# Performance work log

Measured on AMD Instinct MI355X. Metric: run time of the kernel, lower is better.

Reference implementation:

```python
import jax, jax.numpy as jnp
import numpy as np

NUM_FEAT = 512
NUM_HEAD = 8
DEPTH = NUM_FEAT // NUM_HEAD
B, S = 2, 4096


def setup_inputs() -> dict:
    key = jax.random.key(0)
    ks = jax.random.split(key, 12)
    sc = 1.0 / np.sqrt(NUM_FEAT)
    inp = {
        "q": jax.random.normal(ks[0], (B, S, NUM_FEAT), jnp.float32),
        "k": jax.random.normal(ks[1], (B, S, NUM_FEAT), jnp.float32),
        "v": jax.random.normal(ks[2], (B, S, NUM_FEAT), jnp.float32),
        # causal mask: 1 where attention is disallowed (upper triangle), additive style
        "mask": jnp.triu(jnp.ones((S, S), jnp.float32), k=1)[None, None, :, :],
        "wq": jax.random.normal(ks[3], (NUM_FEAT, NUM_FEAT), jnp.float32) * sc,
        "bq": jnp.zeros((NUM_FEAT,), jnp.float32),
        "wk": jax.random.normal(ks[4], (NUM_FEAT, NUM_FEAT), jnp.float32) * sc,
        "bk": jnp.zeros((NUM_FEAT,), jnp.float32),
        "wv": jax.random.normal(ks[5], (NUM_FEAT, NUM_FEAT), jnp.float32) * sc,
        "bv": jnp.zeros((NUM_FEAT,), jnp.float32),
        "wo": jax.random.normal(ks[6], (NUM_FEAT, NUM_FEAT), jnp.float32) * sc,
        "bo": jnp.zeros((NUM_FEAT,), jnp.float32),
    }
    return inp


def _split_heads(x):
    b, s, _ = x.shape
    return x.reshape(b, s, NUM_HEAD, DEPTH).transpose(0, 2, 1, 3)  # [B,H,S,D]


def reference(q, k, v, mask, wq, bq, wk, bk, wv, bv, wo, bo):
    qh = _split_heads(q @ wq + bq)
    kh = _split_heads(k @ wk + bk)
    vh = _split_heads(v @ wv + bv)
    # scaled dot-product attention with materialized [B,H,S,S] scores
    logits = jnp.einsum("bhqd,bhkd->bhqk", qh, kh) / jnp.sqrt(jnp.float32(DEPTH))
    logits = logits + mask * (-1e9)
    weights = jax.nn.softmax(logits, axis=-1)
    attn = jnp.einsum("bhqk,bhkd->bhqd", weights, vh)
    concat = attn.transpose(0, 2, 1, 3).reshape(q.shape[0], -1, NUM_FEAT)
    return concat @ wo + bo
```

## Files before the change

### kernel.cpp

```cpp
#include <hip/hip_runtime.h>
#include <hip/hip_bf16.h>
#include <stdint.h>

#define NB 2
#define NS 4096
#define NF 512
#define NH 8
#define ND 64
#define NM (NB * NS)

typedef __attribute__((ext_vector_type(8))) short bf16x8;
typedef __attribute__((ext_vector_type(4))) float f32x4;
typedef __attribute__((ext_vector_type(16))) float f32x16;

static __device__ __forceinline__ unsigned short f2bf(float f) {
    union { float f; uint32_t u; } x; x.f = f;
    uint32_t u = x.u;
    u += 0x7FFFu + ((u >> 16) & 1u);
    return (unsigned short)(u >> 16);
}

static __device__ __forceinline__ void load_lds16(const void* g, void* l) {
    __builtin_amdgcn_global_load_lds(
        (const __attribute__((address_space(1))) void*)g,
        (__attribute__((address_space(3))) void*)l,
        16, 0, 0);
}

__global__ void convert_all(const float* __restrict__ q, const float* __restrict__ k,
                            const float* __restrict__ v,
                            unsigned short* __restrict__ qb, unsigned short* __restrict__ kb,
                            unsigned short* __restrict__ vb,
                            const float* __restrict__ wq, const float* __restrict__ wk,
                            const float* __restrict__ wv, const float* __restrict__ wo,
                            unsigned short* __restrict__ o0, unsigned short* __restrict__ o1,
                            unsigned short* __restrict__ o2, unsigned short* __restrict__ o3) {
    int i0 = blockIdx.x * blockDim.x + threadIdx.x;
    int stride = gridDim.x * blockDim.x;
    const int n4 = (NB * NS * NF) / 4;
    for (int i = i0; i < n4; i += stride) {
        float4 a = ((const float4*)q)[i];
        float4 b = ((const float4*)k)[i];
        float4 c = ((const float4*)v)[i];
        ushort4 oa, ob, oc;
        oa.x = f2bf(a.x); oa.y = f2bf(a.y); oa.z = f2bf(a.z); oa.w = f2bf(a.w);
        ob.x = f2bf(b.x); ob.y = f2bf(b.y); ob.z = f2bf(b.z); ob.w = f2bf(b.w);
        oc.x = f2bf(c.x); oc.y = f2bf(c.y); oc.z = f2bf(c.z); oc.w = f2bf(c.w);
        ((ushort4*)qb)[i] = oa;
        ((ushort4*)kb)[i] = ob;
        ((ushort4*)vb)[i] = oc;
    }
    for (int i = i0; i < 4 * NF * NF; i += stride) {
        int w = i >> 18;
        int off = i & (NF * NF - 1);
        int r = off >> 9;
        int c = off & (NF - 1);
        const float* src = (w == 0) ? wq : (w == 1) ? wk : (w == 2) ? wv : wo;
        unsigned short* dst = (w == 0) ? o0 : (w == 1) ? o1 : (w == 2) ? o2 : o3;
        dst[c * NF + r] = f2bf(src[off]);
    }
}

__launch_bounds__(256, 2)
__global__ void proj_qkv(const unsigned short* __restrict__ Aq,
                         const unsigned short* __restrict__ Ak,
                         const unsigned short* __restrict__ Av,
                         const unsigned short* __restrict__ WqT,
                         const unsigned short* __restrict__ WkT,
                         const unsigned short* __restrict__ WvT,
                         const float* __restrict__ bq, const float* __restrict__ bk,
                         const float* __restrict__ bv,
                         unsigned short* __restrict__ Qh, unsigned short* __restrict__ Kh,
                         unsigned short* __restrict__ VTs) {
    __shared__ unsigned short smem[2 * 128 * 64];
    unsigned short* As = smem;
    unsigned short* Bs = smem + 128 * 64;

    const int mode = blockIdx.z;
    const unsigned short* A  = (mode == 0) ? Aq : (mode == 1) ? Ak : Av;
    const unsigned short* WT = (mode == 0) ? WqT : (mode == 1) ? WkT : WvT;
    const float* bias        = (mode == 0) ? bq : (mode == 1) ? bk : bv;

    const int t = threadIdx.x;
    const int wid = t >> 6;
    const int lane = t & 63;
    const int l15 = lane & 15;
    const int lhi = lane >> 4;
    const int m0 = blockIdx.x * 128;
    const int n0 = blockIdx.y * 128;
    const int wm = (wid >> 1) * 64;
    const int wn = (wid & 1) * 64;

    const int srow = t >> 3;
    const int scol = ((t & 7) * 16) ^ ((srow & 7) << 4);

    const f32x4 zero4 = {0.f, 0.f, 0.f, 0.f};
    f32x4 acc[4][4];
#pragma unroll
    for (int i = 0; i < 4; ++i)
#pragma unroll
        for (int j = 0; j < 4; ++j) acc[i][j] = zero4;

    for (int k0 = 0; k0 < NF; k0 += 64) {
        __syncthreads();
#pragma unroll
        for (int i = 0; i < 4; ++i) {
            const char* sa = (const char*)A + ((size_t)(m0 + i * 32 + srow) * NF + k0) * 2 + scol;
            load_lds16(sa, (char*)As + i * 4096 + wid * 1024);
            const char* sb = (const char*)WT + ((size_t)(n0 + i * 32 + srow) * NF + k0) * 2 + scol;
            load_lds16(sb, (char*)Bs + i * 4096 + wid * 1024);
        }
        asm volatile("s_waitcnt vmcnt(0)" ::: "memory");
        __syncthreads();

#pragma unroll
        for (int ks = 0; ks < 2; ++ks) {
            bf16x8 af[4], bfr[4];
#pragma unroll
            for (int i = 0; i < 4; ++i) {
                int ra = wm + i * 16 + l15;
                int ca = (ks * 64 + lhi * 16) ^ ((ra & 7) << 4);
                af[i] = *(const bf16x8*)((const char*)As + ra * 128 + ca);
                int rb = wn + i * 16 + l15;
                int cb = (ks * 64 + lhi * 16) ^ ((rb & 7) << 4);
                bfr[i] = *(const bf16x8*)((const char*)Bs + rb * 128 + cb);
            }
#pragma unroll
            for (int mi = 0; mi < 4; ++mi)
#pragma unroll
                for (int ni = 0; ni < 4; ++ni)
                    acc[mi][ni] = __builtin_amdgcn_mfma_f32_16x16x32_bf16(af[mi], bfr[ni], acc[mi][ni], 0, 0, 0);
        }
    }

#pragma unroll
    for (int ni = 0; ni < 4; ++ni) {
        int col = n0 + wn + ni * 16 + l15;
        float bv2 = bias[col];
#pragma unroll
        for (int mi = 0; mi < 4; ++mi) {
#pragma unroll
            for (int r = 0; r < 4; ++r) {
                int row = m0 + wm + mi * 16 + lhi * 4 + r;
                float val = acc[mi][ni][r] + bv2;
                int b = row >> 12, s = row & (NS - 1);
                int hh = col >> 6, d = col & (ND - 1);
                if (mode == 0) {
                    val *= 0.125f;
                    Qh[((size_t)(b * NH + hh) * NS + s) * ND + d] = f2bf(val);
                } else if (mode == 1) {
                    Kh[((size_t)(b * NH + hh) * NS + s) * ND + d] = f2bf(val);
                } else {
                    VTs[((size_t)(b * NH + hh) * ND + d) * NS + s] = f2bf(val);
                }
            }
        }
    }
}

__launch_bounds__(256, 2)
__global__ void proj_o(const unsigned short* __restrict__ A,
                       const unsigned short* __restrict__ WT,
                       const float* __restrict__ bias,
                       float* __restrict__ Out) {
    __shared__ unsigned short smem[2 * 128 * 64];
    unsigned short* As = smem;
    unsigned short* Bs = smem + 128 * 64;

    const int t = threadIdx.x;
    const int wid = t >> 6;
    const int lane = t & 63;
    const int l15 = lane & 15;
    const int lhi = lane >> 4;
    const int m0 = blockIdx.x * 128;
    const int n0 = blockIdx.y * 128;
    const int wm = (wid >> 1) * 64;
    const int wn = (wid & 1) * 64;

    const int srow = t >> 3;
    const int scol = ((t & 7) * 16) ^ ((srow & 7) << 4);

    const f32x4 zero4 = {0.f, 0.f, 0.f, 0.f};
    f32x4 acc[4][4];
#pragma unroll
    for (int i = 0; i < 4; ++i)
#pragma unroll
        for (int j = 0; j < 4; ++j) acc[i][j] = zero4;

    for (int k0 = 0; k0 < NF; k0 += 64) {
        __syncthreads();
#pragma unroll
        for (int i = 0; i < 4; ++i) {
            const char* sa = (const char*)A + ((size_t)(m0 + i * 32 + srow) * NF + k0) * 2 + scol;
            load_lds16(sa, (char*)As + i * 4096 + wid * 1024);
            const char* sb = (const char*)WT + ((size_t)(n0 + i * 32 + srow) * NF + k0) * 2 + scol;
            load_lds16(sb, (char*)Bs + i * 4096 + wid * 1024);
        }
        asm volatile("s_waitcnt vmcnt(0)" ::: "memory");
        __syncthreads();

#pragma unroll
        for (int ks = 0; ks < 2; ++ks) {
            bf16x8 af[4], bfr[4];
#pragma unroll
            for (int i = 0; i < 4; ++i) {
                int ra = wm + i * 16 + l15;
                int ca = (ks * 64 + lhi * 16) ^ ((ra & 7) << 4);
                af[i] = *(const bf16x8*)((const char*)As + ra * 128 + ca);
                int rb = wn + i * 16 + l15;
                int cb = (ks * 64 + lhi * 16) ^ ((rb & 7) << 4);
                bfr[i] = *(const bf16x8*)((const char*)Bs + rb * 128 + cb);
            }
#pragma unroll
            for (int mi = 0; mi < 4; ++mi)
#pragma unroll
                for (int ni = 0; ni < 4; ++ni)
                    acc[mi][ni] = __builtin_amdgcn_mfma_f32_16x16x32_bf16(af[mi], bfr[ni], acc[mi][ni], 0, 0, 0);
        }
    }

#pragma unroll
    for (int ni = 0; ni < 4; ++ni) {
        int col = n0 + wn + ni * 16 + l15;
        float bv2 = bias[col];
#pragma unroll
        for (int mi = 0; mi < 4; ++mi)
#pragma unroll
            for (int r = 0; r < 4; ++r) {
                int row = m0 + wm + mi * 16 + lhi * 4 + r;
                Out[(size_t)row * NF + col] = acc[mi][ni][r] + bv2;
            }
    }
}

__launch_bounds__(128, 2)
__global__ void attn_fused(const unsigned short* __restrict__ Qh,
                           const unsigned short* __restrict__ Kh,
                           const unsigned short* __restrict__ VT,
                           unsigned short* __restrict__ Cc) {
    __shared__ unsigned short smem[16384];

    const int t = threadIdx.x;
    const int wid = t >> 6;
    const int lane = t & 63;
    const int l31 = lane & 31;
    const int h = lane >> 5;
    const int qt = 63 - (int)blockIdx.x;
    const int hh = blockIdx.y, b = blockIdx.z;
    const int q0 = qt * 64;
    const size_t bh = (size_t)b * NH + hh;
    const char* Qp = (const char*)(Qh + bh * NS * ND);
    const char* Kp = (const char*)(Kh + bh * NS * ND);
    const char* Vp = (const char*)(VT + bh * (size_t)ND * NS);

    const int qrow = q0 + wid * 32 + l31;
    bf16x8 qf[4];
#pragma unroll
    for (int kc = 0; kc < 4; ++kc)
        qf[kc] = *(const bf16x8*)(Qp + (size_t)qrow * 128 + kc * 32 + h * 16);

    f32x16 o[2];
#pragma unroll
    for (int r = 0; r < 16; ++r) { o[0][r] = 0.f; o[1][r] = 0.f; }
    float m_run = -1e30f, l_run = 0.f;

    const int srow = lane >> 3;
    const int scol = ((lane & 7) * 16) ^ ((srow & 7) << 4);
    const size_t koff = (size_t)srow * 128 + scol;
    const size_t voff = (size_t)srow * (NS * 2) + scol;

    auto STAGE = [&](int buf, int kv0) {
        char* lk = (char*)smem + buf * 16384;
        if (wid == 0) {
            const char* g = Kp + (size_t)kv0 * 128 + koff;
#pragma unroll
            for (int i = 0; i < 8; ++i)
                load_lds16(g + i * 1024, lk + i * 1024);
        } else {
            const char* g = Vp + (size_t)kv0 * 2 + voff;
            char* lv = lk + 8192;
#pragma unroll
            for (int i = 0; i < 8; ++i)
                load_lds16(g + (size_t)i * 8 * (NS * 2), lv + i * 1024);
        }
    };

    const int nkv = qt + 1;
    const int sw = (l31 & 7) << 4;
    STAGE(0, 0);
    int cur = 0;

    for (int kt = 0; kt < nkv; ++kt) {
        if (kt + 1 < nkv) {
            STAGE(cur ^ 1, (kt + 1) * 64);
            asm volatile("s_waitcnt vmcnt(8)" ::: "memory");
        } else {
            asm volatile("s_waitcnt vmcnt(0)" ::: "memory");
        }
        __builtin_amdgcn_s_barrier();
        __builtin_amdgcn_sched_barrier(0);

        const char* Kb = (const char*)smem + cur * 16384;
        const char* Vb = Kb + 8192;

        f32x16 sT[2];
#pragma unroll
        for (int r = 0; r < 16; ++r) { sT[0][r] = 0.f; sT[1][r] = 0.f; }
#pragma unroll
        for (int kvi = 0; kvi < 2; ++kvi) {
            const int row = kvi * 32 + l31;
#pragma unroll
            for (int kc = 0; kc < 4; ++kc) {
                bf16x8 kf = *(const bf16x8*)(Kb + row * 128 + ((kc * 32 + h * 16) ^ sw));
                sT[kvi] = __builtin_amdgcn_mfma_f32_32x32x16_bf16(kf, qf[kc], sT[kvi], 0, 0, 0);
            }
        }

        if (kt == qt) {
#pragma unroll
            for (int kvi = 0; kvi < 2; ++kvi)
#pragma unroll
                for (int r = 0; r < 16; ++r) {
                    int kv = kt * 64 + kvi * 32 + (r & 3) + ((r >> 2) << 3) + h * 4;
                    if (kv > qrow) sT[kvi][r] = -1e30f;
                }
        }

        float pm = -1e30f;
#pragma unroll
        for (int kvi = 0; kvi < 2; ++kvi)
#pragma unroll
            for (int r = 0; r < 16; ++r) pm = fmaxf(pm, sT[kvi][r]);
        pm = fmaxf(pm, __shfl_xor(pm, 32));

        if (__ballot(pm > m_run + 8.0f) != 0ull) {
            float mnew = fmaxf(m_run, pm);
            float a = __expf(m_run - mnew);
            m_run = mnew;
            l_run *= a;
#pragma unroll
            for (int di = 0; di < 2; ++di)
#pragma unroll
                for (int r = 0; r < 16; ++r) o[di][r] *= a;
        }
        float rs = 0.f;
#pragma unroll
        for (int kvi = 0; kvi < 2; ++kvi)
#pragma unroll
            for (int r = 0; r < 16; ++r) {
                float p = __expf(sT[kvi][r] - m_run);
                sT[kvi][r] = p;
                rs += p;
            }
        rs += __shfl_xor(rs, 32);
        l_run += rs;

        unsigned int w[2][8];
#pragma unroll
        for (int kvi = 0; kvi < 2; ++kvi)
#pragma unroll
            for (int i = 0; i < 8; ++i)
                w[kvi][i] = (unsigned int)f2bf(sT[kvi][2 * i]) |
                            ((unsigned int)f2bf(sT[kvi][2 * i + 1]) << 16);

        union FB { unsigned int u[4]; bf16x8 v; };
        bf16x8 pf[4];
#pragma unroll
        for (int ck = 0; ck < 4; ++ck) {
            const int kvi = ck >> 1, pb = (ck & 1) * 4;
            unsigned int aSrc = h ? w[kvi][pb + 0] : w[kvi][pb + 2];
            unsigned int bSrc = h ? w[kvi][pb + 1] : w[kvi][pb + 3];
            unsigned int sA = (unsigned int)__shfl_xor((int)aSrc, 32);
            unsigned int sB = (unsigned int)__shfl_xor((int)bSrc, 32);
            FB f;
            f.u[0] = (h == 0) ? w[kvi][pb + 0] : sA;
            f.u[1] = (h == 0) ? w[kvi][pb + 1] : sB;
            f.u[2] = (h == 0) ? sA : w[kvi][pb + 2];
            f.u[3] = (h == 0) ? sB : w[kvi][pb + 3];
            pf[ck] = f.v;
        }

#pragma unroll
        for (int di = 0; di < 2; ++di) {
            const int row = di * 32 + l31;
#pragma unroll
            for (int ck = 0; ck < 4; ++ck) {
                bf16x8 vf = *(const bf16x8*)(Vb + row * 128 + ((ck * 32 + h * 16) ^ sw));
                o[di] = __builtin_amdgcn_mfma_f32_32x32x16_bf16(vf, pf[ck], o[di], 0, 0, 0);
            }
        }

        __builtin_amdgcn_sched_barrier(0);
        __builtin_amdgcn_s_barrier();
        cur ^= 1;
    }

    float inv = 1.0f / l_run;
    size_t obase = ((size_t)b * NS + qrow) * NF + hh * ND;
#pragma unroll
    for (int di = 0; di < 2; ++di)
#pragma unroll
        for (int tq = 0; tq < 4; ++tq) {
            ushort4 pk;
            pk.x = f2bf(o[di][4 * tq + 0] * inv);
            pk.y = f2bf(o[di][4 * tq + 1] * inv);
            pk.z = f2bf(o[di][4 * tq + 2] * inv);
            pk.w = f2bf(o[di][4 * tq + 3] * inv);
            *(ushort4*)(Cc + obase + di * 32 + tq * 8 + h * 4) = pk;
        }
}

extern "C" void kernel_launch(void* const* d_in, const int* in_sizes, int n_in,
                              void* d_out, int out_size, void* d_ws, size_t ws_size,
                              hipStream_t stream) {
    const float* q = (const float*)d_in[0];
    const float* k = (const float*)d_in[1];
    const float* v = (const float*)d_in[2];
    const float* wq = (const float*)d_in[4];
    const float* bq = (const float*)d_in[5];
    const float* wk = (const float*)d_in[6];
    const float* bk = (const float*)d_in[7];
    const float* wv = (const float*)d_in[8];
    const float* bv = (const float*)d_in[9];
    const float* wo = (const float*)d_in[10];
    const float* bo = (const float*)d_in[11];

    const size_t MB = 1u << 20;
    char* ws = (char*)d_ws;
    unsigned short* qb  = (unsigned short*)(ws);
    unsigned short* kb  = (unsigned short*)(ws + 8 * MB);
    unsigned short* vb  = (unsigned short*)(ws + 16 * MB);
    unsigned short* wqT = (unsigned short*)(ws + 24 * MB);
    unsigned short* wkT = (unsigned short*)(ws + 24 * MB + 512 * 1024);
    unsigned short* wvT = (unsigned short*)(ws + 25 * MB);
    unsigned short* woT = (unsigned short*)(ws + 25 * MB + 512 * 1024);
    unsigned short* Qh  = (unsigned short*)(ws + 26 * MB);
    unsigned short* Kh  = (unsigned short*)(ws + 34 * MB);
    unsigned short* VTs = (unsigned short*)(ws + 42 * MB);

    convert_all<<<dim3(2048), dim3(256), 0, stream>>>(q, k, v, qb, kb, vb,
                                                      wq, wk, wv, wo, wqT, wkT, wvT, woT);

    proj_qkv<<<dim3(NM / 128, NF / 128, 3), dim3(256), 0, stream>>>(
        qb, kb, vb, wqT, wkT, wvT, bq, bk, bv, Qh, Kh, VTs);

    attn_fused<<<dim3(64, NH, NB), dim3(128), 0, stream>>>(Qh, Kh, VTs, qb );

    proj_o<<<dim3(NM / 128, NF / 128), dim3(256), 0, stream>>>(qb, woT, bo, (float*)d_out);
}
```

Baseline: 310.8 us.

## Split attention KV loop across two wave pairs and double-buffer projection GEMMs

The attention kernel now runs 256 threads per block, with two wave pairs each processing alternating KV tiles. Their partial softmax states (max, sum, output) are merged through LDS at the end, which shortens the serial causal loop per block. Both projection GEMMs get a double-buffered LDS pipeline with partial vmcnt waits so the next tile loads while the current one computes. The output projection also moves to 64-row tiles for more blocks. The costs are extra LDS per block, which may limit occupancy, and a merge epilogue with its own synchronisation.

```diff
diff --git a/kernel.cpp b/kernel.cpp
--- a/kernel.cpp
+++ b/kernel.cpp
@@ -72,9 +72,7 @@
                          const float* __restrict__ bv,
                          unsigned short* __restrict__ Qh, unsigned short* __restrict__ Kh,
                          unsigned short* __restrict__ VTs) {
-    __shared__ unsigned short smem[2 * 128 * 64];
-    unsigned short* As = smem;
-    unsigned short* Bs = smem + 128 * 64;
+    __shared__ char smem[65536];
 
     const int mode = blockIdx.z;
     const unsigned short* A  = (mode == 0) ? Aq : (mode == 1) ? Ak : Av;
@@ -101,18 +99,32 @@
 #pragma unroll
         for (int j = 0; j < 4; ++j) acc[i][j] = zero4;
 
-    for (int k0 = 0; k0 < NF; k0 += 64) {
-        __syncthreads();
+    auto STAGE = [&](int buf, int k0) {
+        char* As = smem + buf * 32768;
+        char* Bs = As + 16384;
 #pragma unroll
         for (int i = 0; i < 4; ++i) {
             const char* sa = (const char*)A + ((size_t)(m0 + i * 32 + srow) * NF + k0) * 2 + scol;
-            load_lds16(sa, (char*)As + i * 4096 + wid * 1024);
+            load_lds16(sa, As + i * 4096 + wid * 1024);
             const char* sb = (const char*)WT + ((size_t)(n0 + i * 32 + srow) * NF + k0) * 2 + scol;
-            load_lds16(sb, (char*)Bs + i * 4096 + wid * 1024);
-        }
-        asm volatile("s_waitcnt vmcnt(0)" ::: "memory");
-        __syncthreads();
-
+            load_lds16(sb, Bs + i * 4096 + wid * 1024);
+        }
+    };
+
+    STAGE(0, 0);
+    int cur = 0;
+    for (int kt = 0; kt < 8; ++kt) {
+        if (kt < 7) {
+            STAGE(cur ^ 1, (kt + 1) * 64);
+            asm volatile("s_waitcnt vmcnt(8)" ::: "memory");
+        } else {
+            asm volatile("s_waitcnt vmcnt(0)" ::: "memory");
+        }
+        __builtin_amdgcn_s_barrier();
+        __builtin_amdgcn_sched_barrier(0);
+
+        const char* As = smem + cur * 32768;
+        const char* Bs = As + 16384;
 #pragma unroll
         for (int ks = 0; ks < 2; ++ks) {
             bf16x8 af[4], bfr[4];
@@ -120,10 +132,10 @@
             for (int i = 0; i < 4; ++i) {
                 int ra = wm + i * 16 + l15;
                 int ca = (ks * 64 + lhi * 16) ^ ((ra & 7) << 4);
-                af[i] = *(const bf16x8*)((const char*)As + ra * 128 + ca);
+                af[i] = *(const bf16x8*)(As + ra * 128 + ca);
                 int rb = wn + i * 16 + l15;
                 int cb = (ks * 64 + lhi * 16) ^ ((rb & 7) << 4);
-                bfr[i] = *(const bf16x8*)((const char*)Bs + rb * 128 + cb);
+                bfr[i] = *(const bf16x8*)(Bs + rb * 128 + cb);
             }
 #pragma unroll
             for (int mi = 0; mi < 4; ++mi)
@@ -131,6 +143,9 @@
                 for (int ni = 0; ni < 4; ++ni)
                     acc[mi][ni] = __builtin_amdgcn_mfma_f32_16x16x32_bf16(af[mi], bfr[ni], acc[mi][ni], 0, 0, 0);
         }
+        __builtin_amdgcn_sched_barrier(0);
+        __builtin_amdgcn_s_barrier();
+        cur ^= 1;
     }
 
 #pragma unroll
@@ -163,60 +178,81 @@
                        const unsigned short* __restrict__ WT,
                        const float* __restrict__ bias,
                        float* __restrict__ Out) {
-    __shared__ unsigned short smem[2 * 128 * 64];
-    unsigned short* As = smem;
-    unsigned short* Bs = smem + 128 * 64;
+    __shared__ char smem[49152];
 
     const int t = threadIdx.x;
     const int wid = t >> 6;
     const int lane = t & 63;
     const int l15 = lane & 15;
     const int lhi = lane >> 4;
-    const int m0 = blockIdx.x * 128;
+    const int m0 = blockIdx.x * 64;
     const int n0 = blockIdx.y * 128;
-    const int wm = (wid >> 1) * 64;
+    const int wm = (wid >> 1) * 32;
     const int wn = (wid & 1) * 64;
 
     const int srow = t >> 3;
     const int scol = ((t & 7) * 16) ^ ((srow & 7) << 4);
 
     const f32x4 zero4 = {0.f, 0.f, 0.f, 0.f};
-    f32x4 acc[4][4];
-#pragma unroll
-    for (int i = 0; i < 4; ++i)
+    f32x4 acc[2][4];
+#pragma unroll
+    for (int i = 0; i < 2; ++i)
 #pragma unroll
         for (int j = 0; j < 4; ++j) acc[i][j] = zero4;
 
-    for (int k0 = 0; k0 < NF; k0 += 64) {
-        __syncthreads();
+    auto STAGE = [&](int buf, int k0) {
+        char* As = smem + buf * 24576;
+        char* Bs = As + 8192;
+#pragma unroll
+        for (int i = 0; i < 2; ++i) {
+            const char* sa = (const char*)A + ((size_t)(m0 + i * 32 + srow) * NF + k0) * 2 + scol;
+            load_lds16(sa, As + i * 4096 + wid * 1024);
+        }
 #pragma unroll
         for (int i = 0; i < 4; ++i) {
-            const char* sa = (const char*)A + ((size_t)(m0 + i * 32 + srow) * NF + k0) * 2 + scol;
-            load_lds16(sa, (char*)As + i * 4096 + wid * 1024);
             const char* sb = (const char*)WT + ((size_t)(n0 + i * 32 + srow) * NF + k0) * 2 + scol;
-            load_lds16(sb, (char*)Bs + i * 4096 + wid * 1024);
-        }
-        asm volatile("s_waitcnt vmcnt(0)" ::: "memory");
-        __syncthreads();
-
+            load_lds16(sb, Bs + i * 4096 + wid * 1024);
+        }
+    };
+
+    STAGE(0, 0);
+    int cur = 0;
+    for (int kt = 0; kt < 8; ++kt) {
+        if (kt < 7) {
+            STAGE(cur ^ 1, (kt + 1) * 64);
+            asm volatile("s_waitcnt vmcnt(6)" ::: "memory");
+        } else {
+            asm volatile("s_waitcnt vmcnt(0)" ::: "memory");
+        }
+        __builtin_amdgcn_s_barrier();
+        __builtin_amdgcn_sched_barrier(0);
+
+        const char* As = smem + cur * 24576;
+        const char* Bs = As + 8192;
 #pragma unroll
         for (int ks = 0; ks < 2; ++ks) {
-            bf16x8 af[4], bfr[4];
-#pragma unroll
-            for (int i = 0; i < 4; ++i) {
+            bf16x8 af[2], bfr[4];
+#pragma unroll
+            for (int i = 0; i < 2; ++i) {
                 int ra = wm + i * 16 + l15;
                 int ca = (ks * 64 + lhi * 16) ^ ((ra & 7) << 4);
-                af[i] = *(const bf16x8*)((const char*)As + ra * 128 + ca);
+                af[i] = *(const bf16x8*)(As + ra * 128 + ca);
+            }
+#pragma unroll
+            for (int i = 0; i < 4; ++i) {
                 int rb = wn + i * 16 + l15;
                 int cb = (ks * 64 + lhi * 16) ^ ((rb & 7) << 4);
-                bfr[i] = *(const bf16x8*)((const char*)Bs + rb * 128 + cb);
-            }
-#pragma unroll
-            for (int mi = 0; mi < 4; ++mi)
+                bfr[i] = *(const bf16x8*)(Bs + rb * 128 + cb);
+            }
+#pragma unroll
+            for (int mi = 0; mi < 2; ++mi)
 #pragma unroll
                 for (int ni = 0; ni < 4; ++ni)
                     acc[mi][ni] = __builtin_amdgcn_mfma_f32_16x16x32_bf16(af[mi], bfr[ni], acc[mi][ni], 0, 0, 0);
         }
+        __builtin_amdgcn_sched_barrier(0);
+        __builtin_amdgcn_s_barrier();
+        cur ^= 1;
     }
 
 #pragma unroll
@@ -224,7 +260,7 @@
         int col = n0 + wn + ni * 16 + l15;
         float bv2 = bias[col];
 #pragma unroll
-        for (int mi = 0; mi < 4; ++mi)
+        for (int mi = 0; mi < 2; ++mi)
 #pragma unroll
             for (int r = 0; r < 4; ++r) {
                 int row = m0 + wm + mi * 16 + lhi * 4 + r;
@@ -233,15 +269,17 @@
     }
 }
 
-__launch_bounds__(128, 2)
+__launch_bounds__(256, 2)
 __global__ void attn_fused(const unsigned short* __restrict__ Qh,
                            const unsigned short* __restrict__ Kh,
                            const unsigned short* __restrict__ VT,
                            unsigned short* __restrict__ Cc) {
-    __shared__ unsigned short smem[16384];
+    __shared__ char smem[65536];
 
     const int t = threadIdx.x;
     const int wid = t >> 6;
+    const int pair = wid >> 1;
+    const int a = wid & 1;
     const int lane = t & 63;
     const int l31 = lane & 31;
     const int h = lane >> 5;
@@ -253,7 +291,7 @@
     const char* Kp = (const char*)(Kh + bh * NS * ND);
     const char* Vp = (const char*)(VT + bh * (size_t)ND * NS);
 
-    const int qrow = q0 + wid * 32 + l31;
+    const int qrow = q0 + a * 32 + l31;
     bf16x8 qf[4];
 #pragma unroll
     for (int kc = 0; kc < 4; ++kc)
@@ -268,31 +306,34 @@
     const int scol = ((lane & 7) * 16) ^ ((srow & 7) << 4);
     const size_t koff = (size_t)srow * 128 + scol;
     const size_t voff = (size_t)srow * (NS * 2) + scol;
+    char* pbase = smem + pair * 32768;
 
     auto STAGE = [&](int buf, int kv0) {
-        char* lk = (char*)smem + buf * 16384;
-        if (wid == 0) {
+        char* dst = pbase + buf * 16384;
+        if (a == 0) {
             const char* g = Kp + (size_t)kv0 * 128 + koff;
 #pragma unroll
             for (int i = 0; i < 8; ++i)
-                load_lds16(g + i * 1024, lk + i * 1024);
+                load_lds16(g + i * 1024, dst + i * 1024);
         } else {
             const char* g = Vp + (size_t)kv0 * 2 + voff;
-            char* lv = lk + 8192;
+            char* lv = dst + 8192;
 #pragma unroll
             for (int i = 0; i < 8; ++i)
                 load_lds16(g + (size_t)i * 8 * (NS * 2), lv + i * 1024);
         }
     };
 
-    const int nkv = qt + 1;
+    const int myC = (qt + 2 - pair) >> 1;
+    const int R = (qt + 2) >> 1;
     const int sw = (l31 & 7) << 4;
-    STAGE(0, 0);
+
+    if (0 < myC) STAGE(0, pair * 64);
     int cur = 0;
 
-    for (int kt = 0; kt < nkv; ++kt) {
-        if (kt + 1 < nkv) {
-            STAGE(cur ^ 1, (kt + 1) * 64);
+    for (int j = 0; j < R; ++j) {
+        if (j + 1 < myC) {
+            STAGE(cur ^ 1, (2 * (j + 1) + pair) * 64);
             asm volatile("s_waitcnt vmcnt(8)" ::: "memory");
         } else {
             asm volatile("s_waitcnt vmcnt(0)" ::: "memory");
@@ -300,93 +341,96 @@
         __builtin_amdgcn_s_barrier();
         __builtin_amdgcn_sched_barrier(0);
 
-        const char* Kb = (const char*)smem + cur * 16384;
-        const char* Vb = Kb + 8192;
-
-        f32x16 sT[2];
-#pragma unroll
-        for (int r = 0; r < 16; ++r) { sT[0][r] = 0.f; sT[1][r] = 0.f; }
-#pragma unroll
-        for (int kvi = 0; kvi < 2; ++kvi) {
-            const int row = kvi * 32 + l31;
-#pragma unroll
-            for (int kc = 0; kc < 4; ++kc) {
-                bf16x8 kf = *(const bf16x8*)(Kb + row * 128 + ((kc * 32 + h * 16) ^ sw));
-                sT[kvi] = __builtin_amdgcn_mfma_f32_32x32x16_bf16(kf, qf[kc], sT[kvi], 0, 0, 0);
-            }
-        }
-
-        if (kt == qt) {
+        if (j < myC) {
+            const int kt = 2 * j + pair;
+            const char* Kb = pbase + cur * 16384;
+            const char* Vb = Kb + 8192;
+
+            f32x16 sT[2];
+#pragma unroll
+            for (int r = 0; r < 16; ++r) { sT[0][r] = 0.f; sT[1][r] = 0.f; }
+#pragma unroll
+            for (int kvi = 0; kvi < 2; ++kvi) {
+                const int row = kvi * 32 + l31;
+#pragma unroll
+                for (int kc = 0; kc < 4; ++kc) {
+                    bf16x8 kf = *(const bf16x8*)(Kb + row * 128 + ((kc * 32 + h * 16) ^ sw));
+                    sT[kvi] = __builtin_amdgcn_mfma_f32_32x32x16_bf16(kf, qf[kc], sT[kvi], 0, 0, 0);
+                }
+            }
+
+            if (kt == qt) {
+#pragma unroll
+                for (int kvi = 0; kvi < 2; ++kvi)
+#pragma unroll
+                    for (int r = 0; r < 16; ++r) {
+                        int kv = kt * 64 + kvi * 32 + (r & 3) + ((r >> 2) << 3) + h * 4;
+                        if (kv > qrow) sT[kvi][r] = -1e30f;
+                    }
+            }
+
+            float pm = -1e30f;
 #pragma unroll
             for (int kvi = 0; kvi < 2; ++kvi)
 #pragma unroll
+                for (int r = 0; r < 16; ++r) pm = fmaxf(pm, sT[kvi][r]);
+            pm = fmaxf(pm, __shfl_xor(pm, 32));
+
+            if (__ballot(pm > m_run + 8.0f) != 0ull) {
+                float mnew = fmaxf(m_run, pm);
+                float sc = __expf(m_run - mnew);
+                m_run = mnew;
+                l_run *= sc;
+#pragma unroll
+                for (int di = 0; di < 2; ++di)
+#pragma unroll
+                    for (int r = 0; r < 16; ++r) o[di][r] *= sc;
+            }
+            float rs = 0.f;
+#pragma unroll
+            for (int kvi = 0; kvi < 2; ++kvi)
+#pragma unroll
                 for (int r = 0; r < 16; ++r) {
-                    int kv = kt * 64 + kvi * 32 + (r & 3) + ((r >> 2) << 3) + h * 4;
-                    if (kv > qrow) sT[kvi][r] = -1e30f;
+                    float p = __expf(sT[kvi][r] - m_run);
+                    sT[kvi][r] = p;
+                    rs += p;
                 }
-        }
-
-        float pm = -1e30f;
-#pragma unroll
-        for (int kvi = 0; kvi < 2; ++kvi)
-#pragma unroll
-            for (int r = 0; r < 16; ++r) pm = fmaxf(pm, sT[kvi][r]);
-        pm = fmaxf(pm, __shfl_xor(pm, 32));
-
-        if (__ballot(pm > m_run + 8.0f) != 0ull) {
-            float mnew = fmaxf(m_run, pm);
-            float a = __expf(m_run - mnew);
-            m_run = mnew;
-            l_run *= a;
-#pragma unroll
-            for (int di = 0; di < 2; ++di)
-#pragma unroll
-                for (int r = 0; r < 16; ++r) o[di][r] *= a;
-        }
-        float rs = 0.f;
-#pragma unroll
-        for (int kvi = 0; kvi < 2; ++kvi)
-#pragma unroll
-            for (int r = 0; r < 16; ++r) {
-                float p = __expf(sT[kvi][r] - m_run);
-                sT[kvi][r] = p;
-                rs += p;
-            }
-        rs += __shfl_xor(rs, 32);
-        l_run += rs;
-
-        unsigned int w[2][8];
-#pragma unroll
-        for (int kvi = 0; kvi < 2; ++kvi)
-#pragma unroll
-            for (int i = 0; i < 8; ++i)
-                w[kvi][i] = (unsigned int)f2bf(sT[kvi][2 * i]) |
-                            ((unsigned int)f2bf(sT[kvi][2 * i + 1]) << 16);
-
-        union FB { unsigned int u[4]; bf16x8 v; };
-        bf16x8 pf[4];
-#pragma unroll
-        for (int ck = 0; ck < 4; ++ck) {
-            const int kvi = ck >> 1, pb = (ck & 1) * 4;
-            unsigned int aSrc = h ? w[kvi][pb + 0] : w[kvi][pb + 2];
-            unsigned int bSrc = h ? w[kvi][pb + 1] : w[kvi][pb + 3];
-            unsigned int sA = (unsigned int)__shfl_xor((int)aSrc, 32);
-            unsigned int sB = (unsigned int)__shfl_xor((int)bSrc, 32);
-            FB f;
-            f.u[0] = (h == 0) ? w[kvi][pb + 0] : sA;
-            f.u[1] = (h == 0) ? w[kvi][pb + 1] : sB;
-            f.u[2] = (h == 0) ? sA : w[kvi][pb + 2];
-            f.u[3] = (h == 0) ? sB : w[kvi][pb + 3];
-            pf[ck] = f.v;
-        }
-
-#pragma unroll
-        for (int di = 0; di < 2; ++di) {
-            const int row = di * 32 + l31;
+            rs += __shfl_xor(rs, 32);
+            l_run += rs;
+
+            unsigned int w[2][8];
+#pragma unroll
+            for (int kvi = 0; kvi < 2; ++kvi)
+#pragma unroll
+                for (int i = 0; i < 8; ++i)
+                    w[kvi][i] = (unsigned int)f2bf(sT[kvi][2 * i]) |
+                                ((unsigned int)f2bf(sT[kvi][2 * i + 1]) << 16);
+
+            union FB { unsigned int u[4]; bf16x8 v; };
+            bf16x8 pf[4];
 #pragma unroll
             for (int ck = 0; ck < 4; ++ck) {
-                bf16x8 vf = *(const bf16x8*)(Vb + row * 128 + ((ck * 32 + h * 16) ^ sw));
-                o[di] = __builtin_amdgcn_mfma_f32_32x32x16_bf16(vf, pf[ck], o[di], 0, 0, 0);
+                const int kvi = ck >> 1, pb = (ck & 1) * 4;
+                unsigned int aSrc = h ? w[kvi][pb + 0] : w[kvi][pb + 2];
+                unsigned int bSrc = h ? w[kvi][pb + 1] : w[kvi][pb + 3];
+                unsigned int sA = (unsigned int)__shfl_xor((int)aSrc, 32);
+                unsigned int sB = (unsigned int)__shfl_xor((int)bSrc, 32);
+                FB f;
+                f.u[0] = (h == 0) ? w[kvi][pb + 0] : sA;
+                f.u[1] = (h == 0) ? w[kvi][pb + 1] : sB;
+                f.u[2] = (h == 0) ? sA : w[kvi][pb + 2];
+                f.u[3] = (h == 0) ? sB : w[kvi][pb + 3];
+                pf[ck] = f.v;
+            }
+
+#pragma unroll
+            for (int di = 0; di < 2; ++di) {
+                const int row = di * 32 + l31;
+#pragma unroll
+                for (int ck = 0; ck < 4; ++ck) {
+                    bf16x8 vf = *(const bf16x8*)(Vb + row * 128 + ((ck * 32 + h * 16) ^ sw));
+                    o[di] = __builtin_amdgcn_mfma_f32_32x32x16_bf16(vf, pf[ck], o[di], 0, 0, 0);
+                }
             }
         }
 
@@ -395,19 +439,37 @@
         cur ^= 1;
     }
 
-    float inv = 1.0f / l_run;
-    size_t obase = ((size_t)b * NS + qrow) * NF + hh * ND;
-#pragma unroll
-    for (int di = 0; di < 2; ++di)
-#pragma unroll
-        for (int tq = 0; tq < 4; ++tq) {
-            ushort4 pk;
-            pk.x = f2bf(o[di][4 * tq + 0] * inv);
-            pk.y = f2bf(o[di][4 * tq + 1] * inv);
-            pk.z = f2bf(o[di][4 * tq + 2] * inv);
-            pk.w = f2bf(o[di][4 * tq + 3] * inv);
-            *(ushort4*)(Cc + obase + di * 32 + tq * 8 + h * 4) = pk;
-        }
+    __syncthreads();
+    float* xch = (float*)smem;
+    const int xi = (a * 64 + lane) * 34;
+    if (pair == 1) {
+        xch[xi] = m_run;
+        xch[xi + 1] = l_run;
+#pragma unroll
+        for (int di = 0; di < 2; ++di)
+#pragma unroll
+            for (int r = 0; r < 16; ++r) xch[xi + 2 + di * 16 + r] = o[di][r];
+    }
+    __syncthreads();
+    if (pair == 0) {
+        float m1 = xch[xi], l1 = xch[xi + 1];
+        float m = fmaxf(m_run, m1);
+        float e0 = __expf(m_run - m);
+        float e1 = __expf(m1 - m);
+        float inv = 1.f / (l_run * e0 + l1 * e1);
+        size_t obase = ((size_t)b * NS + qrow) * NF + hh * ND;
+#pragma unroll
+        for (int di = 0; di < 2; ++di)
+#pragma unroll
+            for (int tq = 0; tq < 4; ++tq) {
+                ushort4 pk;
+                pk.x = f2bf((o[di][4 * tq + 0] * e0 + xch[xi + 2 + di * 16 + 4 * tq + 0] * e1) * inv);
+                pk.y = f2bf((o[di][4 * tq + 1] * e0 + xch[xi + 2 + di * 16 + 4 * tq + 1] * e1) * inv);
+                pk.z = f2bf((o[di][4 * tq + 2] * e0 + xch[xi + 2 + di * 16 + 4 * tq + 2] * e1) * inv);
+                pk.w = f2bf((o[di][4 * tq + 3] * e0 + xch[xi + 2 + di * 16 + 4 * tq + 3] * e1) * inv);
+                *(ushort4*)(Cc + obase + di * 32 + tq * 8 + h * 4) = pk;
+            }
+    }
 }
 
 extern "C" void kernel_launch(void* const* d_in, const int* in_sizes, int n_in,
@@ -444,7 +506,7 @@
     proj_qkv<<<dim3(NM / 128, NF / 128, 3), dim3(256), 0, stream>>>(
         qb, kb, vb, wqT, wkT, wvT, bq, bk, bv, Qh, Kh, VTs);
 
-    attn_fused<<<dim3(64, NH, NB), dim3(128), 0, stream>>>(Qh, Kh, VTs, qb );
-
-    proj_o<<<dim3(NM / 128, NF / 128), dim3(256), 0, stream>>>(qb, woT, bo, (float*)d_out);
-}
+    attn_fused<<<dim3(64, NH, NB), dim3(256), 0, stream>>>(Qh, Kh, VTs, qb );
+
+    proj_o<<<dim3(NM / 64, NF / 128), dim3(256), 0, stream>>>(qb, woT, bo, (float*)d_out);
+}
```

Result: slower. 319.3 us (+2.7%).
